# Performance work log

Measured on AMD Instinct MI355X. Metric: run time of the kernel, lower is better.

Reference implementation:

```python
import jax, jax.numpy as jnp
import numpy as np
from jax import lax


def setup_inputs() -> dict:
    key = jax.random.key(0)
    k1, k2 = jax.random.split(key)
    B, N, D = 4, 4096, 128
    f_s = jax.random.normal(k1, (B, N, D), dtype=jnp.float32)
    f_trans = jax.random.normal(k2, (B, N, D), dtype=jnp.float32)
    return {"f_s": f_s, "f_trans": f_trans}


def reference(f_s, f_trans):
    temp = 10.0
    eps = 1e-8
    B, N, D = f_s.shape
    # pairwise dot products, reused for cosine sim and for the logits ("all")
    dots = jnp.einsum('bnd,bmd->bnm', f_s, f_trans)  # [B,N,M]
    norm_s = jnp.linalg.norm(f_s, axis=-1)       # [B,N]
    norm_t = jnp.linalg.norm(f_trans, axis=-1)   # [B,M]
    # torch.cosine_similarity: dot / max(|x|*|y|, eps)
    sim = dots / jnp.maximum(norm_s[:, :, None] * norm_t[:, None, :], eps)
    # argmax over dim=1 (the N axis) -> index per (b, m)
    idx = jnp.argmax(sim, axis=1)  # [B,M] int
    # gather f_trans rows at those indices (detached in the original via numpy)
    pos_q_trans = lax.stop_gradient(
        jnp.take_along_axis(f_trans, idx[..., None], axis=1))  # [B,M,D]
    pos_logit = jnp.sum(f_s * pos_q_trans, axis=-1) / temp  # [B,N] (N==M)
    pos_exp = jnp.exp(pos_logit)
    # sum_m exp(<f_s_n, f_trans_m>/temp) without materializing [B,N,M,D]
    all_exp = jnp.sum(jnp.exp(dots / temp), axis=-1)  # [B,N]
    ratio = jnp.clip(pos_exp / all_exp, 1e-40)
    loss = jnp.mean(jnp.sum(-jnp.log(ratio), axis=-1) / N)
    return loss
```

## Files before the change

### kernel.cpp

```cpp
#include <hip/hip_runtime.h>
#include <math.h>

#define BB 4
#define NN 4096
#define DD 128
#define BM 128
#define MSPLIT 4
#define NIT 8
#define NTT 32

typedef __attribute__((ext_vector_type(8))) short bf16x8;
typedef __attribute__((ext_vector_type(4))) float f32x4;

__device__ __forceinline__ void mfma_16x16x32_bf16(f32x4& d, bf16x8 a, bf16x8 b) {
  asm volatile("v_mfma_f32_16x16x32_bf16 %0, %1, %2, %0" : "+v"(d) : "v"(a), "v"(b));
}

__device__ __forceinline__ void gload16(const void* g, void* lds) {
  __builtin_amdgcn_global_load_lds(
      (const __attribute__((address_space(1))) void*)g,
      (__attribute__((address_space(3))) void*)lds, 16, 0, 0);
}

__device__ __forceinline__ unsigned short f2b(float x) {
  union { float f; unsigned u; } v; v.f = x;
  unsigned r = v.u + 0x7fffu + ((v.u >> 16) & 1u);
  return (unsigned short)(r >> 16);
}

__global__ __launch_bounds__(256) void k_prep(const float* __restrict__ fs,
                                              const float* __restrict__ ft,
                                              unsigned* __restrict__ outb,
                                              float* __restrict__ inv_norm) {
  int w = threadIdx.x >> 6, lane = threadIdx.x & 63;
  int row = blockIdx.x * 4 + w;
  bool is_s = row < BB * NN;
  const float* src = is_s ? fs + (size_t)row * DD
                          : ft + ((size_t)row - BB * NN) * DD;
  float2 v = ((const float2*)src)[lane];
  float cx = is_s ? v.x : v.x * 0.1f;
  float cy = is_s ? v.y : v.y * 0.1f;
  outb[(size_t)row * 64 + lane] = ((unsigned)f2b(cy) << 16) | f2b(cx);
  if (is_s) {
    float s = v.x * v.x + v.y * v.y;
#pragma unroll
    for (int off = 32; off > 0; off >>= 1) s += __shfl_xor(s, off);
    if (lane == 0) inv_norm[row] = 1.0f / sqrtf(s);
  }
}

__global__ __launch_bounds__(256, 2) void k_main(const unsigned short* __restrict__ fsb,
                                                 const unsigned short* __restrict__ ftb,
                                                 const float* __restrict__ inv_norm,
                                                 float* __restrict__ psum,
                                                 float* __restrict__ pmaxv,
                                                 int* __restrict__ pmaxi) {
  __shared__ __align__(16) char smem[69120];
  char* buf0 = smem;
  char* buf1 = smem + 32768;
  float* colV = (float*)(smem + 65536);
  int*   colI = (int*)(smem + 66560);
  float* rowS = (float*)(smem + 67584);
  float* sInv = (float*)(smem + 68608);

  const int t = threadIdx.x;
  const int tn = blockIdx.x, h = blockIdx.y, b = blockIdx.z;
  const int w = t >> 6, lane = t & 63;
  const int l15 = lane & 15, g = lane >> 4;
  const int wr = w >> 1, wc = w & 1;
  const int rnb = wr * 64 + g * 4;

  const char* gA = (const char*)(fsb + ((size_t)b * NN + (size_t)tn * BM) * DD);
  const char* gBbase = (const char*)(ftb + ((size_t)b * NN + (size_t)h * NIT * BM) * DD);

#pragma unroll
  for (int p = 0; p < 8; p++) {
    int s = p * 256 + t;
    int r = s >> 4, cp = s & 15;
    int gsoff = r * 256 + ((cp ^ (r & 15)) << 4);
    int loff = p * 4096 + w * 1024;
    gload16(gA + gsoff, buf1 + loff);
    gload16(gBbase + gsoff, buf0 + loff);
  }
  if (t < BM) sInv[t] = inv_norm[(size_t)b * NN + (size_t)tn * BM + t];
  __syncthreads();

  bf16x8 af[4][4];
#pragma unroll
  for (int kk = 0; kk < 4; kk++)
#pragma unroll
    for (int fi = 0; fi < 4; fi++) {
      int Ra = wr * 64 + fi * 16 + l15;
      int ca = (kk * 4 + g) ^ l15;
      af[kk][fi] = *(const bf16x8*)(buf1 + Ra * 256 + ca * 16);
    }
  float sv[4][4];
#pragma unroll
  for (int fi = 0; fi < 4; fi++)
#pragma unroll
    for (int j = 0; j < 4; j++) sv[fi][j] = sInv[rnb + fi * 16 + j];
  __syncthreads();

  float rowacc[4][4] = {};
  char* cb = buf0;
  char* nb = buf1;

  for (int it = 0; it < NIT; ++it) {
    if (it + 1 < NIT) {
      const char* gBn = gBbase + (size_t)(it + 1) * (BM * DD * 2);
#pragma unroll
      for (int p = 0; p < 8; p++) {
        int s = p * 256 + t;
        int r = s >> 4, cp = s & 15;
        int gsoff = r * 256 + ((cp ^ (r & 15)) << 4);
        int loff = p * 4096 + w * 1024;
        gload16(gBn + gsoff, nb + loff);
      }
    }
    f32x4 acc[4][4] = {};
#pragma unroll
    for (int kk = 0; kk < 4; kk++) {
      bf16x8 bfr[4];
#pragma unroll
      for (int fj = 0; fj < 4; fj++) {
        int Rb = wc * 64 + fj * 16 + l15;
        int ca = (kk * 4 + g) ^ l15;
        bfr[fj] = *(const bf16x8*)(cb + Rb * 256 + ca * 16);
      }
#pragma unroll
      for (int fi = 0; fi < 4; fi++)
#pragma unroll
        for (int fj = 0; fj < 4; fj++)
          mfma_16x16x32_bf16(acc[fi][fj], af[kk][fi], bfr[fj]);
    }
#pragma unroll
    for (int fi = 0; fi < 4; fi++)
#pragma unroll
      for (int j = 0; j < 4; j++) {
        float s = 0.0f;
#pragma unroll
        for (int fj = 0; fj < 4; fj++) s += __expf(acc[fi][fj][j]);
        rowacc[fi][j] += s;
      }
#pragma unroll
    for (int fj = 0; fj < 4; fj++) {
      float bv = -INFINITY; int bo = 0;
#pragma unroll
      for (int fi = 0; fi < 4; fi++)
#pragma unroll
        for (int j = 0; j < 4; j++) {
          float vv = acc[fi][fj][j] * sv[fi][j];
          if (vv > bv) { bv = vv; bo = fi * 16 + j; }
        }
      int bi = rnb + bo;
#pragma unroll
      for (int off = 16; off <= 32; off <<= 1) {
        float ov = __shfl_xor(bv, off);
        int   oi = __shfl_xor(bi, off);
        if (ov > bv || (ov == bv && oi < bi)) { bv = ov; bi = oi; }
      }
      if (g == 0) {
        int cm = wc * 64 + fj * 16 + l15;
        colV[cm * 2 + wr] = bv;
        colI[cm * 2 + wr] = bi;
      }
    }
    __syncthreads();
    if (t < BM) {
      float v0 = colV[t * 2], v1 = colV[t * 2 + 1];
      int   i0 = colI[t * 2], i1 = colI[t * 2 + 1];
      bool tk = v1 > v0;
      float bv = tk ? v1 : v0;
      int   bi = tk ? i1 : i0;
      int m = (h * NIT + it) * BM + t;
      pmaxv[((size_t)b * NN + m) * NTT + tn] = bv;
      pmaxi[((size_t)b * NN + m) * NTT + tn] = tn * BM + bi;
    }
    __syncthreads();
    char* tmp = cb; cb = nb; nb = tmp;
  }

#pragma unroll
  for (int fi = 0; fi < 4; fi++)
#pragma unroll
    for (int j = 0; j < 4; j++) {
      float s = rowacc[fi][j];
#pragma unroll
      for (int off = 1; off <= 8; off <<= 1) s += __shfl_xor(s, off);
      if (l15 == 0) rowS[(rnb + fi * 16 + j) * 2 + wc] = s;
    }
  __syncthreads();
  if (t < BM)
    psum[((size_t)b * NN + tn * BM + t) * MSPLIT + h] = rowS[t * 2] + rowS[t * 2 + 1];
}

__global__ __launch_bounds__(256) void k_post(const float* __restrict__ fs,
                                              const float* __restrict__ ft,
                                              const float* __restrict__ psum,
                                              const float* __restrict__ pmaxv,
                                              const int* __restrict__ pmaxi,
                                              float* __restrict__ blockpart) {
  __shared__ float part[4];
  int w = threadIdx.x >> 6, lane = threadIdx.x & 63;
  int row = blockIdx.x * 4 + w;
  int b = row >> 12;
  float v = -INFINITY; int i = 0x7fffffff;
  if (lane < NTT) {
    v = pmaxv[(size_t)row * NTT + lane];
    i = pmaxi[(size_t)row * NTT + lane];
  }
#pragma unroll
  for (int off = 16; off > 0; off >>= 1) {
    float ov = __shfl_xor(v, off);
    int   oi = __shfl_xor(i, off);
    if (ov > v || (ov == v && oi < i)) { v = ov; i = oi; }
  }
  int j = __shfl(i, 0);
  float2 a = ((const float2*)(fs + (size_t)row * DD))[lane];
  float2 c = ((const float2*)(ft + ((size_t)b * NN + j) * DD))[lane];
  float s = a.x * c.x + a.y * c.y;
#pragma unroll
  for (int off = 32; off > 0; off >>= 1) s += __shfl_xor(s, off);
  if (lane == 0) {
    float4 ps = *(const float4*)&psum[(size_t)row * MSPLIT];
    float term = logf(ps.x + ps.y + ps.z + ps.w) - s * 0.1f;
    part[w] = fminf(term, 92.103403719761827f);
  }
  __syncthreads();
  if (threadIdx.x == 0)
    blockpart[blockIdx.x] = part[0] + part[1] + part[2] + part[3];
}

__global__ __launch_bounds__(256) void k_final(const float* __restrict__ blockpart,
                                               float* __restrict__ out) {
  __shared__ float red[256];
  float s = 0.0f;
  for (int i = threadIdx.x; i < (BB * NN) / 4; i += 256) s += blockpart[i];
  red[threadIdx.x] = s;
  __syncthreads();
  for (int st = 128; st > 0; st >>= 1) {
    if (threadIdx.x < st) red[threadIdx.x] += red[threadIdx.x + st];
    __syncthreads();
  }
  if (threadIdx.x == 0) out[0] = red[0] * (1.0f / (BB * NN));
}

extern "C" void kernel_launch(void* const* d_in, const int* in_sizes, int n_in,
                              void* d_out, int out_size, void* d_ws, size_t ws_size,
                              hipStream_t stream) {
  const float* fs = (const float*)d_in[0];
  const float* ft = (const float*)d_in[1];
  float* out = (float*)d_out;

  const size_t NE = (size_t)BB * NN * DD;
  unsigned short* fsb = (unsigned short*)d_ws;
  unsigned short* ftb = fsb + NE;
  float* inv_norm = (float*)(ftb + NE);
  float* psum     = inv_norm + (size_t)BB * NN;
  float* pmaxv    = psum + (size_t)BB * NN * MSPLIT;
  int*   pmaxi    = (int*)(pmaxv + (size_t)BB * NN * NTT);
  float* blockpart = (float*)(pmaxi + (size_t)BB * NN * NTT);

  k_prep<<<(2 * BB * NN) / 4, 256, 0, stream>>>(fs, ft, (unsigned*)fsb, inv_norm);
  dim3 g2(NN / BM, MSPLIT, BB);
  k_main<<<g2, 256, 0, stream>>>(fsb, ftb, inv_norm, psum, pmaxv, pmaxi);
  k_post<<<(BB * NN) / 4, 256, 0, stream>>>(fs, ft, psum, pmaxv, pmaxi, blockpart);
  k_final<<<1, 256, 0, stream>>>(blockpart, out);
}
```

Baseline: 60.36 us.

## Retile main kernel to 128x64 tiles with per-wave argmax partials and exp2

Shrinks the per-iteration column tile from 128 to 64 rows of f_trans, doubles the M split to 8, and gives each wave its own 32 rows, so LDS drops to 32KB and four blocks can share a CU. The in-block LDS column-argmax combine and its two barriers per iteration are removed. Each wave now writes its own (value, index) pair as a float2 into a 128-wide partial array, and k_post reduces them. The log2(e)/temp factor is folded into the bf16 conversion so the kernel can use exp2f instead of __expf. The cost is more global partial traffic and less reuse of the B tile within a block.

```diff
diff --git a/kernel.cpp b/kernel.cpp
--- a/kernel.cpp
+++ b/kernel.cpp
@@ -4,10 +4,10 @@
 #define BB 4
 #define NN 4096
 #define DD 128
-#define BM 128
-#define MSPLIT 4
+#define MSPLIT 8
 #define NIT 8
-#define NTT 32
+#define TM 64
+#define NP 128
 
 typedef __attribute__((ext_vector_type(8))) short bf16x8;
 typedef __attribute__((ext_vector_type(4))) float f32x4;
@@ -38,8 +38,9 @@
   const float* src = is_s ? fs + (size_t)row * DD
                           : ft + ((size_t)row - BB * NN) * DD;
   float2 v = ((const float2*)src)[lane];
-  float cx = is_s ? v.x : v.x * 0.1f;
-  float cy = is_s ? v.y : v.y * 0.1f;
+  const float C = 0.14426950408889634f;
+  float cx = is_s ? v.x : v.x * C;
+  float cy = is_s ? v.y : v.y * C;
   outb[(size_t)row * 64 + lane] = ((unsigned)f2b(cy) << 16) | f2b(cx);
   if (is_s) {
     float s = v.x * v.x + v.y * v.y;
@@ -49,110 +50,100 @@
   }
 }
 
-__global__ __launch_bounds__(256, 2) void k_main(const unsigned short* __restrict__ fsb,
+__global__ __launch_bounds__(256, 4) void k_main(const unsigned short* __restrict__ fsb,
                                                  const unsigned short* __restrict__ ftb,
                                                  const float* __restrict__ inv_norm,
                                                  float* __restrict__ psum,
-                                                 float* __restrict__ pmaxv,
-                                                 int* __restrict__ pmaxi) {
-  __shared__ __align__(16) char smem[69120];
-  char* buf0 = smem;
-  char* buf1 = smem + 32768;
-  float* colV = (float*)(smem + 65536);
-  int*   colI = (int*)(smem + 66560);
-  float* rowS = (float*)(smem + 67584);
-  float* sInv = (float*)(smem + 68608);
+                                                 float2* __restrict__ pmaxvi) {
+  __shared__ __align__(16) char smem[32768];
 
   const int t = threadIdx.x;
   const int tn = blockIdx.x, h = blockIdx.y, b = blockIdx.z;
   const int w = t >> 6, lane = t & 63;
   const int l15 = lane & 15, g = lane >> 4;
-  const int wr = w >> 1, wc = w & 1;
-  const int rnb = wr * 64 + g * 4;
-
-  const char* gA = (const char*)(fsb + ((size_t)b * NN + (size_t)tn * BM) * DD);
-  const char* gBbase = (const char*)(ftb + ((size_t)b * NN + (size_t)h * NIT * BM) * DD);
-
-#pragma unroll
-  for (int p = 0; p < 8; p++) {
-    int s = p * 256 + t;
-    int r = s >> 4, cp = s & 15;
-    int gsoff = r * 256 + ((cp ^ (r & 15)) << 4);
-    int loff = p * 4096 + w * 1024;
-    gload16(gA + gsoff, buf1 + loff);
-    gload16(gBbase + gsoff, buf0 + loff);
-  }
-  if (t < BM) sInv[t] = inv_norm[(size_t)b * NN + (size_t)tn * BM + t];
-  __syncthreads();
-
-  bf16x8 af[4][4];
+
+  const int t16 = t >> 4, cp = t & 15;
+  const int srcThr = t16 * 256 + ((cp ^ (t16 & 15)) << 4);
+  const int ldsThr = w * 1024;
+
+  const char* gA = (const char*)(fsb + ((size_t)b * NN + (size_t)tn * 128) * DD);
+  const char* gB0 = (const char*)(ftb + ((size_t)b * NN + (size_t)h * (NIT * TM)) * DD);
+
+#pragma unroll
+  for (int p = 0; p < 8; p++)
+    gload16(gA + p * 4096 + srcThr, smem + p * 4096 + ldsThr);
+  __syncthreads();
+
+  bf16x8 af[4][2];
 #pragma unroll
   for (int kk = 0; kk < 4; kk++)
 #pragma unroll
-    for (int fi = 0; fi < 4; fi++) {
-      int Ra = wr * 64 + fi * 16 + l15;
-      int ca = (kk * 4 + g) ^ l15;
-      af[kk][fi] = *(const bf16x8*)(buf1 + Ra * 256 + ca * 16);
-    }
-  float sv[4][4];
-#pragma unroll
-  for (int fi = 0; fi < 4; fi++)
-#pragma unroll
-    for (int j = 0; j < 4; j++) sv[fi][j] = sInv[rnb + fi * 16 + j];
-  __syncthreads();
-
-  float rowacc[4][4] = {};
-  char* cb = buf0;
-  char* nb = buf1;
+    for (int fi = 0; fi < 2; fi++) {
+      int Ra = w * 32 + fi * 16 + l15;
+      af[kk][fi] = *(const bf16x8*)(smem + Ra * 256 + (((kk * 4 + g) ^ l15) << 4));
+    }
+  float sv[2][4];
+  int rowid[2][4];
+  const float* invb = inv_norm + (size_t)b * NN + tn * 128 + w * 32 + g * 4;
+#pragma unroll
+  for (int fi = 0; fi < 2; fi++)
+#pragma unroll
+    for (int j = 0; j < 4; j++) {
+      sv[fi][j] = invb[fi * 16 + j];
+      rowid[fi][j] = w * 32 + fi * 16 + g * 4 + j;
+    }
+  __syncthreads();
+
+  char* cb = smem;
+  char* nb = smem + 16384;
+
+#pragma unroll
+  for (int p = 0; p < 4; p++)
+    gload16(gB0 + p * 4096 + srcThr, cb + p * 4096 + ldsThr);
+
+  float rowacc[2][4] = {};
 
   for (int it = 0; it < NIT; ++it) {
+    __syncthreads();
     if (it + 1 < NIT) {
-      const char* gBn = gBbase + (size_t)(it + 1) * (BM * DD * 2);
-#pragma unroll
-      for (int p = 0; p < 8; p++) {
-        int s = p * 256 + t;
-        int r = s >> 4, cp = s & 15;
-        int gsoff = r * 256 + ((cp ^ (r & 15)) << 4);
-        int loff = p * 4096 + w * 1024;
-        gload16(gBn + gsoff, nb + loff);
-      }
-    }
-    f32x4 acc[4][4] = {};
+      const char* gBn = gB0 + (size_t)(it + 1) * (TM * DD * 2);
+#pragma unroll
+      for (int p = 0; p < 4; p++)
+        gload16(gBn + p * 4096 + srcThr, nb + p * 4096 + ldsThr);
+    }
+    f32x4 acc[2][4] = {};
 #pragma unroll
     for (int kk = 0; kk < 4; kk++) {
       bf16x8 bfr[4];
 #pragma unroll
       for (int fj = 0; fj < 4; fj++) {
-        int Rb = wc * 64 + fj * 16 + l15;
-        int ca = (kk * 4 + g) ^ l15;
-        bfr[fj] = *(const bf16x8*)(cb + Rb * 256 + ca * 16);
-      }
-#pragma unroll
-      for (int fi = 0; fi < 4; fi++)
+        int Rb = fj * 16 + l15;
+        bfr[fj] = *(const bf16x8*)(cb + Rb * 256 + (((kk * 4 + g) ^ l15) << 4));
+      }
+#pragma unroll
+      for (int fi = 0; fi < 2; fi++)
 #pragma unroll
         for (int fj = 0; fj < 4; fj++)
           mfma_16x16x32_bf16(acc[fi][fj], af[kk][fi], bfr[fj]);
     }
 #pragma unroll
-    for (int fi = 0; fi < 4; fi++)
+    for (int fi = 0; fi < 2; fi++)
 #pragma unroll
       for (int j = 0; j < 4; j++) {
-        float s = 0.0f;
-#pragma unroll
-        for (int fj = 0; fj < 4; fj++) s += __expf(acc[fi][fj][j]);
+        float s = (exp2f(acc[fi][0][j]) + exp2f(acc[fi][1][j])) +
+                  (exp2f(acc[fi][2][j]) + exp2f(acc[fi][3][j]));
         rowacc[fi][j] += s;
       }
 #pragma unroll
     for (int fj = 0; fj < 4; fj++) {
-      float bv = -INFINITY; int bo = 0;
-#pragma unroll
-      for (int fi = 0; fi < 4; fi++)
+      float bv = -INFINITY; int bi = 0x7fffffff;
+#pragma unroll
+      for (int fi = 0; fi < 2; fi++)
 #pragma unroll
         for (int j = 0; j < 4; j++) {
           float vv = acc[fi][fj][j] * sv[fi][j];
-          if (vv > bv) { bv = vv; bo = fi * 16 + j; }
+          if (vv > bv) { bv = vv; bi = rowid[fi][j]; }
         }
-      int bi = rnb + bo;
 #pragma unroll
       for (int off = 16; off <= 32; off <<= 1) {
         float ov = __shfl_xor(bv, off);
@@ -160,70 +151,60 @@
         if (ov > bv || (ov == bv && oi < bi)) { bv = ov; bi = oi; }
       }
       if (g == 0) {
-        int cm = wc * 64 + fj * 16 + l15;
-        colV[cm * 2 + wr] = bv;
-        colI[cm * 2 + wr] = bi;
-      }
-    }
-    __syncthreads();
-    if (t < BM) {
-      float v0 = colV[t * 2], v1 = colV[t * 2 + 1];
-      int   i0 = colI[t * 2], i1 = colI[t * 2 + 1];
-      bool tk = v1 > v0;
-      float bv = tk ? v1 : v0;
-      int   bi = tk ? i1 : i0;
-      int m = (h * NIT + it) * BM + t;
-      pmaxv[((size_t)b * NN + m) * NTT + tn] = bv;
-      pmaxi[((size_t)b * NN + m) * NTT + tn] = tn * BM + bi;
-    }
-    __syncthreads();
+        int m = (h * NIT + it) * TM + fj * 16 + l15;
+        float2 pr; pr.x = bv; pr.y = __int_as_float(tn * 128 + bi);
+        pmaxvi[((size_t)b * NN + m) * NP + tn * 4 + w] = pr;
+      }
+    }
     char* tmp = cb; cb = nb; nb = tmp;
   }
 
 #pragma unroll
-  for (int fi = 0; fi < 4; fi++)
+  for (int fi = 0; fi < 2; fi++)
 #pragma unroll
     for (int j = 0; j < 4; j++) {
       float s = rowacc[fi][j];
 #pragma unroll
       for (int off = 1; off <= 8; off <<= 1) s += __shfl_xor(s, off);
-      if (l15 == 0) rowS[(rnb + fi * 16 + j) * 2 + wc] = s;
-    }
-  __syncthreads();
-  if (t < BM)
-    psum[((size_t)b * NN + tn * BM + t) * MSPLIT + h] = rowS[t * 2] + rowS[t * 2 + 1];
+      if (l15 == 0) {
+        int n = tn * 128 + w * 32 + fi * 16 + g * 4 + j;
+        psum[((size_t)b * NN + n) * MSPLIT + h] = s;
+      }
+    }
 }
 
 __global__ __launch_bounds__(256) void k_post(const float* __restrict__ fs,
                                               const float* __restrict__ ft,
                                               const float* __restrict__ psum,
-                                              const float* __restrict__ pmaxv,
-                                              const int* __restrict__ pmaxi,
+                                              const float2* __restrict__ pmaxvi,
                                               float* __restrict__ blockpart) {
   __shared__ float part[4];
   int w = threadIdx.x >> 6, lane = threadIdx.x & 63;
   int row = blockIdx.x * 4 + w;
   int b = row >> 12;
-  float v = -INFINITY; int i = 0x7fffffff;
-  if (lane < NTT) {
-    v = pmaxv[(size_t)row * NTT + lane];
-    i = pmaxi[(size_t)row * NTT + lane];
-  }
-#pragma unroll
-  for (int off = 16; off > 0; off >>= 1) {
+  const float2* pp = pmaxvi + (size_t)row * NP;
+  float2 p0 = pp[lane], p1 = pp[lane + 64];
+  float v = p0.x; int i = __float_as_int(p0.y);
+  {
+    int i1 = __float_as_int(p1.y);
+    if (p1.x > v || (p1.x == v && i1 < i)) { v = p1.x; i = i1; }
+  }
+#pragma unroll
+  for (int off = 32; off > 0; off >>= 1) {
     float ov = __shfl_xor(v, off);
     int   oi = __shfl_xor(i, off);
     if (ov > v || (ov == v && oi < i)) { v = ov; i = oi; }
   }
-  int j = __shfl(i, 0);
   float2 a = ((const float2*)(fs + (size_t)row * DD))[lane];
-  float2 c = ((const float2*)(ft + ((size_t)b * NN + j) * DD))[lane];
+  float2 c = ((const float2*)(ft + ((size_t)b * NN + i) * DD))[lane];
   float s = a.x * c.x + a.y * c.y;
 #pragma unroll
   for (int off = 32; off > 0; off >>= 1) s += __shfl_xor(s, off);
   if (lane == 0) {
-    float4 ps = *(const float4*)&psum[(size_t)row * MSPLIT];
-    float term = logf(ps.x + ps.y + ps.z + ps.w) - s * 0.1f;
+    const float4* ps4 = (const float4*)&psum[(size_t)row * MSPLIT];
+    float4 q0 = ps4[0], q1 = ps4[1];
+    float tot = ((q0.x + q0.y) + (q0.z + q0.w)) + ((q1.x + q1.y) + (q1.z + q1.w));
+    float term = logf(tot) - s * 0.1f;
     part[w] = fminf(term, 92.103403719761827f);
   }
   __syncthreads();
@@ -255,15 +236,14 @@
   const size_t NE = (size_t)BB * NN * DD;
   unsigned short* fsb = (unsigned short*)d_ws;
   unsigned short* ftb = fsb + NE;
-  float* inv_norm = (float*)(ftb + NE);
-  float* psum     = inv_norm + (size_t)BB * NN;
-  float* pmaxv    = psum + (size_t)BB * NN * MSPLIT;
-  int*   pmaxi    = (int*)(pmaxv + (size_t)BB * NN * NTT);
-  float* blockpart = (float*)(pmaxi + (size_t)BB * NN * NTT);
+  float*  inv_norm = (float*)(ftb + NE);
+  float*  psum     = inv_norm + (size_t)BB * NN;
+  float2* pmaxvi   = (float2*)(psum + (size_t)BB * NN * MSPLIT);
+  float*  blockpart = (float*)(pmaxvi + (size_t)BB * NN * NP);
 
   k_prep<<<(2 * BB * NN) / 4, 256, 0, stream>>>(fs, ft, (unsigned*)fsb, inv_norm);
-  dim3 g2(NN / BM, MSPLIT, BB);
-  k_main<<<g2, 256, 0, stream>>>(fsb, ftb, inv_norm, psum, pmaxv, pmaxi);
-  k_post<<<(BB * NN) / 4, 256, 0, stream>>>(fs, ft, psum, pmaxv, pmaxi, blockpart);
+  dim3 g2(NN / 128, MSPLIT, BB);
+  k_main<<<g2, 256, 0, stream>>>(fsb, ftb, inv_norm, psum, pmaxvi);
+  k_post<<<(BB * NN) / 4, 256, 0, stream>>>(fs, ft, psum, pmaxvi, blockpart);
   k_final<<<1, 256, 0, stream>>>(blockpart, out);
 }
```

Result: slower. 65.76 us (+9.0%).
